# Optimization experiments

Hardware: AMD Instinct MI355X
Metric: run time of the kernel (lower is better)

The kernel has to match this reference:

```python
import jax, jax.numpy as jnp
import numpy as np

# static config (matches init_kwargs)
P = 16          # proj_patch_dim (window size)
F = 128         # fmap_dim
NH = F // P     # windows per side = 8
N = P * P       # tokens per window = 256
H = 8           # attn_heads
A = 32          # attn_dim (head dim)
C = 32          # leff_filters_out (channels)
INNER = 128     # leff_filters
B = 8           # batch
EPS = 1e-5

# relative-position index (static)
_c = np.stack(np.meshgrid(np.arange(P), np.arange(P), indexing='ij'))  # [2,P,P]
_f = _c.reshape(2, -1)                                                  # [2,N]
_r = _f[:, :, None] - _f[:, None, :]                                    # [2,N,N]
_rpi = (_r[0] + P - 1) * (2 * P - 1) + (_r[1] + P - 1)                  # [N,N]
RPI = jnp.asarray(_rpi.reshape(-1))

# shifted-window attention mask (static)
_sm = np.zeros((F, F), np.float32)
_cnt = 0
_slices = (slice(0, -P), slice(-P, -P // 2), slice(-P // 2, None))
for _hs in _slices:
    for _ws in _slices:
        _sm[_hs, _ws] = _cnt
        _cnt += 1
_smw = _sm.reshape(NH, P, NH, P).transpose(0, 2, 1, 3).reshape(NH * NH, N)
_am = _smw[:, None, :] - _smw[:, :, None]
_am = np.where(_am != 0, np.float32(-100.0), np.float32(0.0))
SHIFT_MASK = jnp.asarray(_am.reshape(1, NH * NH, 1, N, N))


def _ln(x, g, b):
    m = jnp.mean(x, axis=-1, keepdims=True)
    v = jnp.var(x, axis=-1, keepdims=True)
    return (x - m) / jnp.sqrt(v + EPS) * g + b


def setup_inputs() -> dict:
    key = jax.random.key(0)
    ks = jax.random.split(key, 16)
    s = 0.02
    return {
        'x': jax.random.normal(ks[0], (B, F * F, C), jnp.float32),
        'norm1_g': jnp.ones((C,), jnp.float32),
        'norm1_b': jnp.zeros((C,), jnp.float32),
        'mod_w': jax.random.normal(ks[1], (N, C), jnp.float32) * s,
        'qkv_w': jax.random.normal(ks[2], (C, 3 * H * A), jnp.float32) * s,
        'qkv_b': jnp.zeros((3 * H * A,), jnp.float32),
        'rpbt': jax.random.normal(ks[3], ((2 * P - 1) ** 2, H), jnp.float32) * s,
        'rev_w': jax.random.normal(ks[4], (H * A, C), jnp.float32) * s,
        'rev_b': jnp.zeros((C,), jnp.float32),
        'norm2_g': jnp.ones((C,), jnp.float32),
        'norm2_b': jnp.zeros((C,), jnp.float32),
        'lp1_w': jax.random.normal(ks[5], (C, INNER), jnp.float32) * s,
        'lp1_b': jnp.zeros((INNER,), jnp.float32),
        'conv_w': jax.random.normal(ks[6], (3, 3, INNER, INNER), jnp.float32) * s,  # HWIO
        'conv_b': jnp.zeros((INNER,), jnp.float32),
        'lp2_w': jax.random.normal(ks[7], (INNER, C), jnp.float32) * s,
        'lp2_b': jnp.zeros((C,), jnp.float32),
    }


def reference(x, norm1_g, norm1_b, mod_w, qkv_w, qkv_b, rpbt, rev_w, rev_b,
              norm2_g, norm2_b, lp1_w, lp1_b, conv_w, conv_b, lp2_w, lp2_b):
    shortcut = x
    h = _ln(x, norm1_g, norm1_b)
    h = h.reshape(B, F, F, C)
    h = jnp.roll(h, (-P // 2, -P // 2), axis=(1, 2))          # cyclic shift
    # window partition: [B*NH*NH, N, C]
    h = h.reshape(B, NH, P, NH, P, C).transpose(0, 1, 3, 2, 4, 5).reshape(B * NH * NH, N, C)
    h = h + mod_w                                              # learned modulator
    qkv = h @ qkv_w + qkv_b                                    # [W, N, 3*H*A]
    qkv = qkv.reshape(-1, N, 3, H, A).transpose(2, 0, 3, 1, 4) # [3, W, H, N, A]
    q = qkv[0] * (A ** -0.5)
    k = qkv[1]
    v = qkv[2]
    attn = jnp.einsum('whna,whma->whnm', q, k)                 # [W, H, N, N]
    rpb = rpbt[RPI].reshape(N, N, H).transpose(2, 0, 1)        # [H, N, N]
    attn = attn + rpb[None]
    attn = attn.reshape(B, NH * NH, H, N, N) + SHIFT_MASK
    attn = attn.reshape(-1, H, N, N)
    attn = jax.nn.softmax(attn, axis=-1)
    o = jnp.einsum('whnm,whma->whna', attn, v)                 # [W, H, N, A]
    o = o.transpose(0, 2, 1, 3).reshape(-1, N, H * A)
    o = o @ rev_w + rev_b                                      # [W, N, C]
    # window reverse + reverse cyclic shift
    o = o.reshape(B, NH, NH, P, P, C).transpose(0, 1, 3, 2, 4, 5).reshape(B, F, F, C)
    o = jnp.roll(o, (P // 2, P // 2), axis=(1, 2)).reshape(B, F * F, C)
    x_res = shortcut + o
    # LeFF
    y = _ln(x_res, norm2_g, norm2_b)
    y = jax.nn.gelu(y @ lp1_w + lp1_b, approximate=False)
    y = y.reshape(B, F, F, INNER)
    y = jax.lax.conv_general_dilated(y, conv_w, (1, 1), 'SAME',
                                     dimension_numbers=('NHWC', 'HWIO', 'NHWC')) + conv_b
    y = jax.nn.gelu(y, approximate=False)
    y = y.reshape(B, F * F, INNER)
    y = jax.nn.gelu(y @ lp2_w + lp2_b, approximate=False)
    return y + x_res
```

## Files before the change

kernel.cpp:

```cpp
#include <hip/hip_runtime.h>
#include <math.h>

#define Fdim 128
#define Pw   16
#define Hh   8
#define Cc   32
#define Bb   8

typedef short  short8  __attribute__((ext_vector_type(8)));
typedef float  floatx4 __attribute__((ext_vector_type(4)));

#define QSCL   0.2550348637f
#define MASKC2 (-144.26950408889634f)

__device__ __forceinline__ float gelu_f(float x){
    return 0.5f * x * (1.0f + erff(x * 0.70710678118654752f));
}
__device__ __forceinline__ unsigned pk2(float a, float b){
    unsigned ua = __builtin_bit_cast(unsigned, a) + 0x8000u;
    unsigned ub = __builtin_bit_cast(unsigned, b) + 0x8000u;
    return __builtin_amdgcn_perm(ub, ua, 0x07060302);
}
__device__ __forceinline__ unsigned pk2t(float a, float b){
    return __builtin_amdgcn_perm(__builtin_bit_cast(unsigned, b),
                                 __builtin_bit_cast(unsigned, a), 0x07060302);
}
__device__ __forceinline__ short bf16s(float a){
    return (short)((__builtin_bit_cast(unsigned, a) + 0x8000u) >> 16);
}
__device__ __forceinline__ float hi2f(unsigned d){ return __builtin_bit_cast(float, d & 0xffff0000u); }
__device__ __forceinline__ float lo2f(unsigned d){ return __builtin_bit_cast(float, d << 16); }

__global__ __launch_bounds__(256) void prep_kernel(
    const float* __restrict__ qkv_w, const float* __restrict__ rev_w,
    const float* __restrict__ rpbt,  const float* __restrict__ lp1_w,
    const float* __restrict__ conv_w, const float* __restrict__ lp2_w,
    const float* __restrict__ qkv_b, const float* __restrict__ rev_b,
    short* __restrict__ qkv_wT, short* __restrict__ rev_wT, unsigned* __restrict__ rplb,
    short* __restrict__ lp1_wT, short* __restrict__ conv_wT, short* __restrict__ lp2_wT,
    short* __restrict__ wvr, float* __restrict__ rbtot)
{
    int i = blockIdx.x * 256 + threadIdx.x;
    if (i < 24576){
        int col = i >> 5, c = i & 31;
        qkv_wT[i] = bf16s(qkv_w[c*768 + col]);
    } else if (i < 32768){
        int j = i - 24576;
        int h = j >> 10, r = j & 1023;
        int c = r >> 5, a = r & 31;
        rev_wT[j] = bf16s(rev_w[(h*32 + a)*32 + c]);
    } else if (i < 40464){
        int j = i - 32768;
        int h = j / 962, d = j % 962;
        int g0 = (d < 481) ? (2*d) : (2*(d-481) + 1);
        float f0 = (g0     < 961) ? rpbt[g0*8 + h]*1.4426950408889634f : 0.f;
        float f1 = (g0 + 1 < 961) ? rpbt[(g0+1)*8 + h]*1.4426950408889634f : 0.f;
        rplb[j] = pk2(f0, f1);
    } else if (i < 44560){
        int j = i - 40464;
        int f = j >> 5, c = j & 31;
        lp1_wT[j] = bf16s(lp1_w[c*128 + f]);
    } else if (i < 192016){
        int j = i - 44560;
        int ci_in = j & 7;
        int co    = (j >> 3) & 127;
        int chk   = (j >> 10) & 3;
        int s     = j >> 12;
        int tap = s % 9, kc = s / 9;
        conv_wT[j] = bf16s(conv_w[(tap*128 + kc*32 + chk*8 + ci_in)*128 + co]);
    } else if (i < 196112){
        int j = i - 192016;
        int oc = j >> 7, co = j & 127;
        lp2_wT[j] = bf16s(lp2_w[co*32 + oc]);
    } else if (i < 204304){
        int j  = i - 196112;
        int h  = j >> 10, aa = (j >> 5) & 31, c = j & 31;
        float s = 0.f;
        for (int a = 0; a < 32; a++)
            s += qkv_w[c*768 + 512 + h*32 + a] * rev_w[(h*32 + a)*32 + aa];
        wvr[j] = bf16s(s);
    } else if (i < 204336){
        int aa = i - 204304;
        float s = rev_b[aa];
        for (int m = 0; m < 256; m++)
            s += qkv_b[512 + m] * rev_w[m*32 + aa];
        rbtot[aa] = s;
    }
}

__global__
__attribute__((amdgpu_flat_work_group_size(512,512), amdgpu_waves_per_eu(4,4)))
void attn_kernel(
    const float* __restrict__ x,   const float* __restrict__ n1g,
    const float* __restrict__ n1b, const float* __restrict__ mod_w,
    const float* __restrict__ qkv_b, const float* __restrict__ rbtot,
    const short* __restrict__ qkv_wT, const short* __restrict__ wvr,
    const unsigned* __restrict__ rplb,
    float* __restrict__ x_res)
{
    __shared__ __align__(16) short hmodS[4*256*8];
    __shared__ __align__(16) short Kbuf[256*40];
    __shared__ __align__(16) short Qbuf[256*40];
    __shared__ __align__(16) short VTb[32*264];
    __shared__ __align__(16) unsigned rplbS[962];
    __shared__ unsigned regnp[64];

    const int w  = blockIdx.x;
    const int b  = w >> 6;
    const int wi = w & 63;
    const int wh = wi >> 3, ww = wi & 7;
    const int tid  = threadIdx.x;
    const int wv   = tid >> 6;
    const int ln   = tid & 63;
    const int quad = ln >> 4;
    const int l15  = ln & 15;
    const bool masked = (wh == 7) || (ww == 7);

    if (tid < 256){
        const int n  = tid;
        const int rn = n >> 4, cn = n & 15;
        const int gh = (wh*Pw + rn + 8) & 127;
        const int gw = (ww*Pw + cn + 8) & 127;
        const float* xr = x + (((size_t)b << 14) + (gh << 7) + gw) * Cc;
        float v[Cc];
        const float4* x4 = reinterpret_cast<const float4*>(xr);
        float4* v4 = reinterpret_cast<float4*>(v);
        #pragma unroll
        for (int i = 0; i < Cc/4; i++) v4[i] = x4[i];
        float mean = 0.f;
        #pragma unroll
        for (int c = 0; c < Cc; c++) mean += v[c];
        mean *= (1.0f/Cc);
        float var = 0.f;
        #pragma unroll
        for (int c = 0; c < Cc; c++){ float d = v[c] - mean; var = fmaf(d, d, var); }
        var *= (1.0f/Cc);
        const float rinv = rsqrtf(var + 1e-5f);
        #pragma unroll
        for (int c = 0; c < Cc; c++)
            v[c] = (v[c] - mean)*rinv*n1g[c] + n1b[c] + mod_w[n*Cc + c];
        #pragma unroll
        for (int i = 0; i < 4; i++){
            uint4 dw;
            dw.x = pk2(v[8*i+0], v[8*i+1]);
            dw.y = pk2(v[8*i+2], v[8*i+3]);
            dw.z = pk2(v[8*i+4], v[8*i+5]);
            dw.w = pk2(v[8*i+6], v[8*i+7]);
            *(uint4*)(&hmodS[i*2048 + n*8]) = dw;
        }
    }
    if (tid < 64){
        int rm  = tid >> 2;
        int shm = wh*Pw + rm;
        int hreg = (shm < 112) ? 0 : ((shm < 120) ? 1 : 2);
        unsigned dw = 0;
        #pragma unroll
        for (int i = 0; i < 4; i++){
            int cm  = (tid & 3)*4 + i;
            int swm = ww*Pw + cm;
            int wreg = (swm < 112) ? 0 : ((swm < 120) ? 1 : 2);
            dw |= (unsigned)(hreg*3 + wreg) << (8*i);
        }
        regnp[tid] = dw;
    }
    __syncthreads();

    unsigned regq[2] = {0,0};
    if (masked){
        #pragma unroll
        for (int nt = 0; nt < 2; nt++){
            int q = wv*32 + nt*16 + l15;
            regq[nt] = (regnp[q >> 2] >> ((q & 3)*8)) & 255u;
        }
    }

    floatx4 RV[2][2];
    #pragma unroll
    for (int cm = 0; cm < 2; cm++)
        #pragma unroll
        for (int nt = 0; nt < 2; nt++)
            RV[cm][nt] = (floatx4){0.f,0.f,0.f,0.f};

    const int s0lane = 12 + l15 - 4*quad;
    const floatx4 zz = (floatx4){0.f,0.f,0.f,0.f};
    const short8 ONEv = {0x3F80,0x3F80,0x3F80,0x3F80,0x3F80,0x3F80,0x3F80,0x3F80};

    for (int h = 0; h < Hh; h++){
        __syncthreads();

        #pragma unroll
        for (int k2 = 0; k2 < 2; k2++){
            int i = k2*512 + tid;
            if (i < 962) rplbS[i] = rplb[h*962 + i];
        }

        short8 HF[2];
        #pragma unroll
        for (int ii = 0; ii < 2; ii++)
            HF[ii] = *(const short8*)(&hmodS[quad*2048 + (wv*32 + ii*16 + l15)*8]);
        short8 WQ[2], WK[2], WVb[2];
        float4 bq[2], bk[2];
        #pragma unroll
        for (int mt = 0; mt < 2; mt++){
            WQ[mt]  = *(const short8*)(qkv_wT + (      h*32 + mt*16 + l15)*32 + quad*8);
            WK[mt]  = *(const short8*)(qkv_wT + (256 + h*32 + mt*16 + l15)*32 + quad*8);
            WVb[mt] = *(const short8*)(wvr    + (      h*32 + mt*16 + l15)*32 + quad*8);
            bq[mt]  = *(const float4*)(qkv_b +       h*32 + mt*16 + quad*4);
            bk[mt]  = *(const float4*)(qkv_b + 256 + h*32 + mt*16 + quad*4);
        }
        #pragma unroll
        for (int ii = 0; ii < 2; ii++){
            const int tok = wv*32 + ii*16;
            #pragma unroll
            for (int mt = 0; mt < 2; mt++){
                floatx4 qf = __builtin_amdgcn_mfma_f32_16x16x32_bf16(WQ[mt], HF[ii], zz, 0,0,0);
                floatx4 kf = __builtin_amdgcn_mfma_f32_16x16x32_bf16(WK[mt], HF[ii], zz, 0,0,0);
                floatx4 vf = __builtin_amdgcn_mfma_f32_16x16x32_bf16(HF[ii], WVb[mt], zz, 0,0,0);
                uint2 qv;
                qv.x = pk2((qf[0]+bq[mt].x)*QSCL, (qf[1]+bq[mt].y)*QSCL);
                qv.y = pk2((qf[2]+bq[mt].z)*QSCL, (qf[3]+bq[mt].w)*QSCL);
                *(uint2*)(&Qbuf[(tok + l15)*40 + mt*16 + quad*4]) = qv;
                uint2 kv;
                kv.x = pk2(kf[0]+bk[mt].x, kf[1]+bk[mt].y);
                kv.y = pk2(kf[2]+bk[mt].z, kf[3]+bk[mt].w);
                *(uint2*)(&Kbuf[(tok + l15)*40 + mt*16 + quad*4]) = kv;
                uint2 vv;
                vv.x = pk2(vf[0], vf[1]);
                vv.y = pk2(vf[2], vf[3]);
                *(uint2*)(&VTb[(mt*16 + l15)*264 + tok + quad*4]) = vv;
            }
        }
        __syncthreads();

        short8 QB[2];
        #pragma unroll
        for (int nt = 0; nt < 2; nt++)
            QB[nt] = *(const short8*)(&Qbuf[(wv*32 + nt*16 + l15)*40 + quad*8]);

        floatx4 OT[2][2];
        #pragma unroll
        for (int am = 0; am < 2; am++)
            #pragma unroll
            for (int nt = 0; nt < 2; nt++)
                OT[am][nt] = (floatx4){0.f,0.f,0.f,0.f};
        floatx4 RS[2] = {zz, zz};

        for (int ch = 0; ch < 8; ch++){
            short8 KA[2];
            KA[0] = *(const short8*)(&Kbuf[(ch*32 +      l15)*40 + quad*8]);
            KA[1] = *(const short8*)(&Kbuf[(ch*32 + 16 + l15)*40 + quad*8]);

            unsigned pd0[3], pd1[3];
            int base = wv*2 - ch*2;
            #pragma unroll
            for (int j = 0; j < 3; j++){
                int dt  = base + j - 1;
                int g0  = (dt + 15)*31 + s0lane;
                int dwi = (g0 & 1) ? (481 + (g0 >> 1)) : (g0 >> 1);
                pd0[j] = rplbS[dwi];
                pd1[j] = rplbS[dwi + 1];
            }
            unsigned rk[2] = {0,0};
            if (masked){
                rk[0] = regnp[ch*8 +     quad];
                rk[1] = regnp[ch*8 + 4 + quad];
            }

            #pragma unroll
            for (int sub = 0; sub < 2; sub++){
                #pragma unroll
                for (int nt = 0; nt < 2; nt++){
                    int j = nt - sub + 1;
                    floatx4 ci;
                    ci[0] = hi2f(pd1[j]); ci[1] = lo2f(pd1[j]);
                    ci[2] = hi2f(pd0[j]); ci[3] = lo2f(pd0[j]);
                    if (masked){
                        ci[0] += (((rk[sub]      ) & 255u) == regq[nt]) ? 0.f : MASKC2;
                        ci[1] += (((rk[sub] >>  8) & 255u) == regq[nt]) ? 0.f : MASKC2;
                        ci[2] += (((rk[sub] >> 16) & 255u) == regq[nt]) ? 0.f : MASKC2;
                        ci[3] += (((rk[sub] >> 24) & 255u) == regq[nt]) ? 0.f : MASKC2;
                    }
                    floatx4 S = __builtin_amdgcn_mfma_f32_16x16x32_bf16(KA[sub], QB[nt], ci, 0,0,0);
                    float p0 = __builtin_amdgcn_exp2f(S[0]);
                    float p1 = __builtin_amdgcn_exp2f(S[1]);
                    float p2 = __builtin_amdgcn_exp2f(S[2]);
                    float p3 = __builtin_amdgcn_exp2f(S[3]);
                    uint2 pv; pv.x = pk2t(p0, p1); pv.y = pk2t(p2, p3);
                    *(uint2*)(&Qbuf[(wv*32 + nt*16 + l15)*40 + sub*16 + quad*4]) = pv;
                }
            }

            short8 VA0 = *(const short8*)(&VTb[(     l15)*264 + ch*32 + quad*8]);
            short8 VA1 = *(const short8*)(&VTb[(16 + l15)*264 + ch*32 + quad*8]);
            #pragma unroll
            for (int nt = 0; nt < 2; nt++){
                short8 PB = *(const short8*)(&Qbuf[(wv*32 + nt*16 + l15)*40 + quad*8]);
                OT[0][nt] = __builtin_amdgcn_mfma_f32_16x16x32_bf16(VA0, PB, OT[0][nt], 0,0,0);
                OT[1][nt] = __builtin_amdgcn_mfma_f32_16x16x32_bf16(VA1, PB, OT[1][nt], 0,0,0);
                RS[nt]    = __builtin_amdgcn_mfma_f32_16x16x32_bf16(ONEv, PB, RS[nt], 0,0,0);
            }
        }

        float inv[2];
        inv[0] = 1.0f / RS[0][0];
        inv[1] = 1.0f / RS[1][0];
        #pragma unroll
        for (int am = 0; am < 2; am++)
            #pragma unroll
            for (int nt = 0; nt < 2; nt++){
                floatx4 o = OT[am][nt];
                float iv = inv[nt];
                RV[am][nt][0] = fmaf(o[0], iv, RV[am][nt][0]);
                RV[am][nt][1] = fmaf(o[1], iv, RV[am][nt][1]);
                RV[am][nt][2] = fmaf(o[2], iv, RV[am][nt][2]);
                RV[am][nt][3] = fmaf(o[3], iv, RV[am][nt][3]);
            }
    }

    #pragma unroll
    for (int cm = 0; cm < 2; cm++){
        float4 rb = *(const float4*)(rbtot + cm*16 + quad*4);
        #pragma unroll
        for (int nt = 0; nt < 2; nt++){
            int gh = (wh*Pw + wv*2 + nt + 8) & 127;
            int gw = (ww*Pw + l15 + 8) & 127;
            size_t gaddr = (((size_t)b << 14) + (gh << 7) + gw)*Cc + cm*16 + quad*4;
            float4 xv = *(const float4*)(x + gaddr);
            floatx4 o = RV[cm][nt];
            float4 ov;
            ov.x = xv.x + rb.x + o[0];
            ov.y = xv.y + rb.y + o[1];
            ov.z = xv.z + rb.z + o[2];
            ov.w = xv.w + rb.w + o[3];
            *(float4*)(x_res + gaddr) = ov;
        }
    }
}

__global__
__attribute__((amdgpu_flat_work_group_size(512,512), amdgpu_waves_per_eu(4,4)))
void leff_kernel(
    const float* __restrict__ x_res, const float* __restrict__ n2g,
    const float* __restrict__ n2b,  const float* __restrict__ lp1_b,
    const float* __restrict__ conv_b, const float* __restrict__ lp2_b,
    const short* __restrict__ lp1_wT, const short* __restrict__ conv_wT,
    const short* __restrict__ lp2_wT, float* __restrict__ out)
{
    __shared__ __align__(16) char lds[70144];
    short* xa   = (short*)lds;
    short* y1c  = (short*)(lds + 26880);
    short* wbuf = (short*)(lds + 53760);
    short* y2   = (short*)lds;

    const int blk = blockIdx.x;
    const int b   = blk >> 6;
    const int ty  = (blk >> 3) & 7, tx = blk & 7;
    const int tid  = threadIdx.x;
    const int wv   = tid >> 6;
    const int ln   = tid & 63;
    const int quad = ln >> 4;
    const int l15  = ln & 15;
    const floatx4 zz = (floatx4){0.f,0.f,0.f,0.f};

    if (tid < 336){
        int hp = tid;
        int hy = hp / 18, hx = hp - hy*18;
        int gy = ty*16 + hy - 1, gx = tx*16 + hx - 1;
        bool ok = (hp < 324) && ((unsigned)gy < 128u) && ((unsigned)gx < 128u);
        if (ok){
            const float* xr = x_res + (((size_t)b << 14) + (gy << 7) + gx)*Cc;
            float v[Cc];
            const float4* x4 = reinterpret_cast<const float4*>(xr);
            float4* v4 = reinterpret_cast<float4*>(v);
            #pragma unroll
            for (int i = 0; i < Cc/4; i++) v4[i] = x4[i];
            float mean = 0.f;
            #pragma unroll
            for (int c = 0; c < Cc; c++) mean += v[c];
            mean *= (1.0f/Cc);
            float var = 0.f;
            #pragma unroll
            for (int c = 0; c < Cc; c++){ float d = v[c] - mean; var = fmaf(d, d, var); }
            var *= (1.0f/Cc);
            const float rinv = rsqrtf(var + 1e-5f);
            #pragma unroll
            for (int i = 0; i < 4; i++){
                float w0 = (v[8*i+0]-mean)*rinv*n2g[8*i+0] + n2b[8*i+0];
                float w1 = (v[8*i+1]-mean)*rinv*n2g[8*i+1] + n2b[8*i+1];
                float w2 = (v[8*i+2]-mean)*rinv*n2g[8*i+2] + n2b[8*i+2];
                float w3 = (v[8*i+3]-mean)*rinv*n2g[8*i+3] + n2b[8*i+3];
                float w4 = (v[8*i+4]-mean)*rinv*n2g[8*i+4] + n2b[8*i+4];
                float w5 = (v[8*i+5]-mean)*rinv*n2g[8*i+5] + n2b[8*i+5];
                float w6 = (v[8*i+6]-mean)*rinv*n2g[8*i+6] + n2b[8*i+6];
                float w7 = (v[8*i+7]-mean)*rinv*n2g[8*i+7] + n2b[8*i+7];
                uint4 dw;
                dw.x = pk2(w0,w1); dw.y = pk2(w2,w3);
                dw.z = pk2(w4,w5); dw.w = pk2(w6,w7);
                *(uint4*)(xa + hp*40 + i*8) = dw;
            }
        } else {
            uint4 z = {0,0,0,0};
            #pragma unroll
            for (int i = 0; i < 4; i++) *(uint4*)(xa + hp*40 + i*8) = z;
        }
    }

    ((uint4*)wbuf)[tid] = ((const uint4*)conv_wT)[tid];

    floatx4 acc[2][8];
    #pragma unroll
    for (int j = 0; j < 2; j++)
        #pragma unroll
        for (int m = 0; m < 8; m++) acc[j][m] = zz;

    for (int idx = 0; idx < 36; idx++){
        const int kc  = idx / 9;
        const int tap = idx - kc*9;

        if (tap == 0){
            __syncthreads();
            short8 A1[2]; float4 b1[2];
            #pragma unroll
            for (int mt = 0; mt < 2; mt++){
                A1[mt] = *(const short8*)(lp1_wT + (kc*32 + mt*16 + l15)*32 + quad*8);
                b1[mt] = *(const float4*)(lp1_b + kc*32 + mt*16 + quad*4);
            }
            #pragma unroll
            for (int ii = 0; ii < 3; ii++){
                int nt = wv + 8*ii;
                if (nt < 21){
                    int px = nt*16 + l15;
                    int hy = px / 18, hx = px - hy*18;
                    int gy = ty*16 + hy - 1, gx = tx*16 + hx - 1;
                    bool oob = (px >= 324) || ((unsigned)gy > 127u) || ((unsigned)gx > 127u);
                    short8 Bx = *(const short8*)(xa + px*40 + quad*8);
                    #pragma unroll
                    for (int mt = 0; mt < 2; mt++){
                        floatx4 c = __builtin_amdgcn_mfma_f32_16x16x32_bf16(A1[mt], Bx, zz, 0,0,0);
                        float v0 = oob ? 0.f : gelu_f(c[0] + b1[mt].x);
                        float v1 = oob ? 0.f : gelu_f(c[1] + b1[mt].y);
                        float v2 = oob ? 0.f : gelu_f(c[2] + b1[mt].z);
                        float v3 = oob ? 0.f : gelu_f(c[3] + b1[mt].w);
                        uint2 pv; pv.x = pk2(v0, v1); pv.y = pk2(v2, v3);
                        *(uint2*)(y1c + px*40 + mt*16 + quad*4) = pv;
                    }
                }
            }
        }

        uint4 pf;
        if (idx < 35) pf = ((const uint4*)conv_wT)[(idx + 1)*512 + tid];

        __syncthreads();

        const short* wb = wbuf + (idx & 1)*4096;
        const int ky = tap / 3, kx = tap - ky*3;

        short8 Bf[2];
        #pragma unroll
        for (int j = 0; j < 2; j++){
            int oy = wv*2 + j;
            int hp = (oy + ky)*18 + kx + l15;
            Bf[j] = *(const short8*)(y1c + hp*40 + quad*8);
        }
        #pragma unroll
        for (int m = 0; m < 8; m++){
            short8 Aw = *(const short8*)(wb + quad*1024 + (m*16 + l15)*8);
            acc[0][m] = __builtin_amdgcn_mfma_f32_16x16x32_bf16(Aw, Bf[0], acc[0][m], 0,0,0);
            acc[1][m] = __builtin_amdgcn_mfma_f32_16x16x32_bf16(Aw, Bf[1], acc[1][m], 0,0,0);
        }

        if (idx < 35)
            ((uint4*)(wbuf + ((idx + 1) & 1)*4096))[tid] = pf;
    }

    __syncthreads();

    #pragma unroll
    for (int j = 0; j < 2; j++){
        int px = (wv*2 + j)*16 + l15;
        #pragma unroll
        for (int m = 0; m < 8; m++){
            float4 cb = *(const float4*)(conv_b + m*16 + quad*4);
            floatx4 a = acc[j][m];
            float v0 = gelu_f(a[0] + cb.x);
            float v1 = gelu_f(a[1] + cb.y);
            float v2 = gelu_f(a[2] + cb.z);
            float v3 = gelu_f(a[3] + cb.w);
            uint2 pv; pv.x = pk2(v0, v1); pv.y = pk2(v2, v3);
            *(uint2*)(y2 + px*136 + m*16 + quad*4) = pv;
        }
    }
    __syncthreads();

    short8 A2[2][4]; float4 lb[2];
    #pragma unroll
    for (int mt = 0; mt < 2; mt++){
        #pragma unroll
        for (int k = 0; k < 4; k++)
            A2[mt][k] = *(const short8*)(lp2_wT + (mt*16 + l15)*128 + k*32 + quad*8);
        lb[mt] = *(const float4*)(lp2_b + mt*16 + quad*4);
    }
    #pragma unroll
    for (int j = 0; j < 2; j++){
        int oy = wv*2 + j;
        floatx4 c2[2] = {zz, zz};
        #pragma unroll
        for (int k = 0; k < 4; k++){
            short8 Bf = *(const short8*)(y2 + (oy*16 + l15)*136 + k*32 + quad*8);
            c2[0] = __builtin_amdgcn_mfma_f32_16x16x32_bf16(A2[0][k], Bf, c2[0], 0,0,0);
            c2[1] = __builtin_amdgcn_mfma_f32_16x16x32_bf16(A2[1][k], Bf, c2[1], 0,0,0);
        }
        int gy = ty*16 + oy, gx = tx*16 + l15;
        size_t base = (((size_t)b << 14) + (gy << 7) + gx)*Cc;
        #pragma unroll
        for (int mt = 0; mt < 2; mt++){
            size_t ad = base + mt*16 + quad*4;
            float4 xr = *(const float4*)(x_res + ad);
            float4 ov;
            ov.x = gelu_f(c2[mt][0] + lb[mt].x) + xr.x;
            ov.y = gelu_f(c2[mt][1] + lb[mt].y) + xr.y;
            ov.z = gelu_f(c2[mt][2] + lb[mt].z) + xr.z;
            ov.w = gelu_f(c2[mt][3] + lb[mt].w) + xr.w;
            *(float4*)(out + ad) = ov;
        }
    }
}

extern "C" void kernel_launch(void* const* d_in, const int* in_sizes, int n_in,
                              void* d_out, int out_size, void* d_ws, size_t ws_size,
                              hipStream_t stream)
{
    (void)in_sizes; (void)n_in; (void)out_size; (void)ws_size;
    const float* x      = (const float*)d_in[0];
    const float* n1g    = (const float*)d_in[1];
    const float* n1b    = (const float*)d_in[2];
    const float* mod_w  = (const float*)d_in[3];
    const float* qkv_w  = (const float*)d_in[4];
    const float* qkv_b  = (const float*)d_in[5];
    const float* rpbt   = (const float*)d_in[6];
    const float* rev_w  = (const float*)d_in[7];
    const float* rev_b  = (const float*)d_in[8];
    const float* n2g    = (const float*)d_in[9];
    const float* n2b    = (const float*)d_in[10];
    const float* lp1_w  = (const float*)d_in[11];
    const float* lp1_b  = (const float*)d_in[12];
    const float* conv_w = (const float*)d_in[13];
    const float* conv_b = (const float*)d_in[14];
    const float* lp2_w  = (const float*)d_in[15];
    const float* lp2_b  = (const float*)d_in[16];
    float* out = (float*)d_out;

    char* wsb = (char*)d_ws;
    float*    x_res  = (float*)wsb;
    short*    qkv_wT = (short*)(wsb + 16777216);
    short*    rev_wT = (short*)(wsb + 16826368);
    unsigned* rplbT  = (unsigned*)(wsb + 16842752);
    short*    lp1_wT = (short*)(wsb + 16873536);
    short*    conv_wT= (short*)(wsb + 16881728);
    short*    lp2_wT = (short*)(wsb + 17176640);
    short*    wvrT   = (short*)(wsb + 17184832);
    float*    rbtot  = (float*)(wsb + 17201216);

    prep_kernel<<<799, 256, 0, stream>>>(qkv_w, rev_w, rpbt, lp1_w, conv_w, lp2_w,
                                         qkv_b, rev_b,
                                         qkv_wT, rev_wT, rplbT, lp1_wT, conv_wT, lp2_wT,
                                         wvrT, rbtot);
    attn_kernel<<<512, 512, 0, stream>>>(x, n1g, n1b, mod_w, qkv_b, rbtot,
                                         qkv_wT, wvrT, rplbT, x_res);
    leff_kernel<<<512, 512, 0, stream>>>(x_res, n2g, n2b, lp1_b, conv_b, lp2_b,
                                         lp1_wT, conv_wT, lp2_wT, out);
}
```

Baseline: 250.7 us.

## Batch three conv taps per LDS weight stage to cut barriers in LeFF

```diff
diff --git a/kernel.cpp b/kernel.cpp
--- a/kernel.cpp
+++ b/kernel.cpp
@@ -346,7 +346,7 @@
     const short* __restrict__ lp1_wT, const short* __restrict__ conv_wT,
     const short* __restrict__ lp2_wT, float* __restrict__ out)
 {
-    __shared__ __align__(16) char lds[70144];
+    __shared__ __align__(16) char lds[78336];
     short* xa   = (short*)lds;
     short* y1c  = (short*)(lds + 26880);
     short* wbuf = (short*)(lds + 53760);
@@ -405,7 +405,9 @@
         }
     }
 
-    ((uint4*)wbuf)[tid] = ((const uint4*)conv_wT)[tid];
+    uint4 pf0 = ((const uint4*)conv_wT)[tid];
+    uint4 pf1 = ((const uint4*)conv_wT)[512  + tid];
+    uint4 pf2 = ((const uint4*)conv_wT)[1024 + tid];
 
     floatx4 acc[2][8];
     #pragma unroll
@@ -413,12 +415,12 @@
         #pragma unroll
         for (int m = 0; m < 8; m++) acc[j][m] = zz;
 
-    for (int idx = 0; idx < 36; idx++){
-        const int kc  = idx / 9;
-        const int tap = idx - kc*9;
-
-        if (tap == 0){
-            __syncthreads();
+    for (int g = 0; g < 12; g++){
+        const int gm3 = g - (g/3)*3;
+        __syncthreads();
+
+        if (gm3 == 0){
+            const int kc = g / 3;
             short8 A1[2]; float4 b1[2];
             #pragma unroll
             for (int mt = 0; mt < 2; mt++){
@@ -448,30 +450,35 @@
             }
         }
 
-        uint4 pf;
-        if (idx < 35) pf = ((const uint4*)conv_wT)[(idx + 1)*512 + tid];
-
+        ((uint4*)wbuf)[tid]        = pf0;
+        ((uint4*)wbuf)[512  + tid] = pf1;
+        ((uint4*)wbuf)[1024 + tid] = pf2;
         __syncthreads();
 
-        const short* wb = wbuf + (idx & 1)*4096;
-        const int ky = tap / 3, kx = tap - ky*3;
-
-        short8 Bf[2];
-        #pragma unroll
-        for (int j = 0; j < 2; j++){
-            int oy = wv*2 + j;
-            int hp = (oy + ky)*18 + kx + l15;
-            Bf[j] = *(const short8*)(y1c + hp*40 + quad*8);
-        }
-        #pragma unroll
-        for (int m = 0; m < 8; m++){
-            short8 Aw = *(const short8*)(wb + quad*1024 + (m*16 + l15)*8);
-            acc[0][m] = __builtin_amdgcn_mfma_f32_16x16x32_bf16(Aw, Bf[0], acc[0][m], 0,0,0);
-            acc[1][m] = __builtin_amdgcn_mfma_f32_16x16x32_bf16(Aw, Bf[1], acc[1][m], 0,0,0);
-        }
-
-        if (idx < 35)
-            ((uint4*)(wbuf + ((idx + 1) & 1)*4096))[tid] = pf;
+        if (g < 11){
+            pf0 = ((const uint4*)conv_wT)[(g+1)*1536 +        tid];
+            pf1 = ((const uint4*)conv_wT)[(g+1)*1536 + 512  + tid];
+            pf2 = ((const uint4*)conv_wT)[(g+1)*1536 + 1024 + tid];
+        }
+
+        const int ky = gm3;
+        #pragma unroll
+        for (int t = 0; t < 3; t++){
+            const short* wb = wbuf + t*4096;
+            short8 Bf[2];
+            #pragma unroll
+            for (int j = 0; j < 2; j++){
+                int oy = wv*2 + j;
+                int hp = (oy + ky)*18 + t + l15;
+                Bf[j] = *(const short8*)(y1c + hp*40 + quad*8);
+            }
+            #pragma unroll
+            for (int m = 0; m < 8; m++){
+                short8 Aw = *(const short8*)(wb + quad*1024 + (m*16 + l15)*8);
+                acc[0][m] = __builtin_amdgcn_mfma_f32_16x16x32_bf16(Aw, Bf[0], acc[0][m], 0,0,0);
+                acc[1][m] = __builtin_amdgcn_mfma_f32_16x16x32_bf16(Aw, Bf[1], acc[1][m], 0,0,0);
+            }
+        }
     }
 
     __syncthreads();
```

Result: slower. 288.9 us (+15.2%).
